# Performance work log

Hardware: AMD Instinct MI355X
Metric: run time of the kernel (lower is better)

## Reference

```python
import jax, jax.numpy as jnp
import numpy as np

N_NODES = 2048
N_FLUID = 400000
N_SOLID = 400000


def setup_inputs() -> dict:
    key = jax.random.key(0)
    k1, k2, k3 = jax.random.split(key, 3)
    nodes = jax.random.uniform(k1, (N_NODES, 3), dtype=jnp.float32)
    # sorted distinct node ids per tet: sort 4 draws from [0, N-4) then add offsets 0..3
    fe = jnp.sort(jax.random.randint(k2, (N_FLUID, 4), 0, N_NODES - 4), axis=1) + jnp.arange(4)
    se = jnp.sort(jax.random.randint(k3, (N_SOLID, 4), 0, N_NODES - 4), axis=1) + jnp.arange(4)
    return {
        "nodes": nodes,
        "fluid_elements": fe.astype(jnp.int32),
        "solid_elements": se.astype(jnp.int32),
        "E_mod": jnp.float32(2.1e11),
        "nu": jnp.float32(0.3),
        "rho_s": jnp.float32(7850.0),
    }


def _grads_and_volume(coords):
    """coords: [E,4,3] -> shape-fn gradients [E,4,3], volume [E]."""
    ones = jnp.ones(coords.shape[:-1] + (1,), coords.dtype)
    A = jnp.concatenate([ones, coords], axis=-1)
    A_inv = jnp.linalg.inv(A)
    grads = jnp.swapaxes(A_inv[..., 1:, :], -1, -2)        # [E,4,3]
    v0 = coords[:, 1] - coords[:, 0]
    v1 = coords[:, 2] - coords[:, 0]
    v2 = coords[:, 3] - coords[:, 0]
    vol = jnp.abs(jnp.linalg.det(jnp.stack([v0, v1, v2], axis=-1))) / 6.0  # [E]
    return grads, vol


def _fluid_element_matrices(coords):
    grads, vol = _grads_and_volume(coords)
    K_e = vol[:, None, None] * jnp.einsum("eik,ejk->eij", grads, grads)      # [E,4,4]
    m_template = (2.0 * jnp.eye(4, dtype=coords.dtype) + jnp.ones((4, 4), coords.dtype)) / 10.0
    M_e = vol[:, None, None] * m_template
    return K_e, M_e


def _elasticity_D(E_mod, nu):
    coeff = E_mod / ((1.0 + nu) * (1.0 - 2.0 * nu))
    top = nu * jnp.ones((3, 3), jnp.float32) + (1.0 - 2.0 * nu) * jnp.eye(3, dtype=jnp.float32)
    D = jnp.zeros((6, 6), jnp.float32)
    D = D.at[:3, :3].set(top)
    D = D.at[3:, 3:].set(((1.0 - 2.0 * nu) / 2.0) * jnp.eye(3, dtype=jnp.float32))
    return coeff * D


def _solid_element_matrices(coords, E_mod, nu, rho_s):
    grads, vol = _grads_and_volume(coords)                 # grads [E,4,3]
    bx, by, bz = grads[..., 0], grads[..., 1], grads[..., 2]   # each [E,4]
    z = jnp.zeros_like(bx)
    # per-node 6x3 strain-displacement block -> [E,4,6,3]
    block = jnp.stack([
        jnp.stack([bx, z, z], axis=-1),
        jnp.stack([z, by, z], axis=-1),
        jnp.stack([z, z, bz], axis=-1),
        jnp.stack([by, bx, z], axis=-1),
        jnp.stack([z, bz, by], axis=-1),
        jnp.stack([bz, z, bx], axis=-1),
    ], axis=-2)
    E = coords.shape[0]
    B = jnp.transpose(block, (0, 2, 1, 3)).reshape(E, 6, 12)  # [E,6,12]
    D = _elasticity_D(E_mod, nu)                              # [6,6]
    K_e = vol[:, None, None] * jnp.einsum("eai,ab,ebj->eij", B, D, B)  # [E,12,12]
    M_e = (rho_s * vol / 4.0)[:, None, None] * jnp.eye(12, dtype=coords.dtype)
    return K_e, M_e


def reference(nodes, fluid_elements, solid_elements, E_mod, nu, rho_s):
    n = nodes.shape[0]
    # ---- fluid: local matrices + scatter-add assembly into [N,N] ----
    cf = nodes[fluid_elements]                              # [Ef,4,3]
    Kf_e, Mf_e = _fluid_element_matrices(cf)
    rows = fluid_elements[:, :, None]                       # [Ef,4,1]
    cols = fluid_elements[:, None, :]                       # [Ef,1,4]
    K_f = jnp.zeros((n, n), jnp.float32).at[rows, cols].add(Kf_e)
    M_f = jnp.zeros((n, n), jnp.float32).at[rows, cols].add(Mf_e)
    # ---- solid: 3 dof/node, assembly into [3N,3N] ----
    cs = nodes[solid_elements]                              # [Es,4,3]
    Ks_e, Ms_e = _solid_element_matrices(cs, E_mod, nu, rho_s)
    dofs = (3 * solid_elements[:, :, None] + jnp.arange(3)).reshape(solid_elements.shape[0], 12)
    K_s = jnp.zeros((3 * n, 3 * n), jnp.float32).at[dofs[:, :, None], dofs[:, None, :]].add(Ks_e)
    M_s = jnp.zeros((3 * n, 3 * n), jnp.float32).at[dofs[:, :, None], dofs[:, None, :]].add(Ms_e)
    return (K_f, M_f, K_s, M_s)
```

## Files before the change

kernel.cpp:

```cpp
#include <hip/hip_runtime.h>


#define G_PART 256
#define BT 512
#define GW (BT / 64)
#define TCAP 1024
#define NCPT 4
#define VSTRIDE 13

__device__ __forceinline__ float sel4(float x0, float x1, float x2, float x3, int a) {
    float r = x0;
    r = (a == 1) ? x1 : r;
    r = (a == 2) ? x2 : r;
    r = (a == 3) ? x3 : r;
    return r;
}
__device__ __forceinline__ int sel4i(int x0, int x1, int x2, int x3, int a) {
    int r = x0;
    r = (a == 1) ? x1 : r;
    r = (a == 2) ? x2 : r;
    r = (a == 3) ? x3 : r;
    return r;
}

__device__ __forceinline__ float wave_reduce(float v) {
#pragma unroll
    for (int m = 1; m < 64; m <<= 1) v += __shfl_xor(v, m, 64);
    return v;
}

__device__ __forceinline__ void tet_geom_f(const float* __restrict__ nodes,
                                           int n0, int n1, int n2, int n3_,
                                           float& gx1, float& gy1, float& gz1,
                                           float& gx2, float& gy2, float& gz2,
                                           float& gx3, float& gy3, float& gz3,
                                           float& volf)
{
    const float* q0 = nodes + 3ll * n0;
    const float* q1 = nodes + 3ll * n1;
    const float* q2 = nodes + 3ll * n2;
    const float* q3 = nodes + 3ll * n3_;
    double p0x = q0[0], p0y = q0[1], p0z = q0[2];
    double r1x = (double)q1[0] - p0x, r1y = (double)q1[1] - p0y, r1z = (double)q1[2] - p0z;
    double r2x = (double)q2[0] - p0x, r2y = (double)q2[1] - p0y, r2z = (double)q2[2] - p0z;
    double r3x = (double)q3[0] - p0x, r3y = (double)q3[1] - p0y, r3z = (double)q3[2] - p0z;
    double c23x = r2y*r3z - r2z*r3y, c23y = r2z*r3x - r2x*r3z, c23z = r2x*r3y - r2y*r3x;
    double det = r1x*c23x + r1y*c23y + r1z*c23z;
    double inv = 1.0 / det;
    double c31x = r3y*r1z - r3z*r1y, c31y = r3z*r1x - r3x*r1z, c31z = r3x*r1y - r3y*r1x;
    double c12x = r1y*r2z - r1z*r2y, c12y = r1z*r2x - r1x*r2z, c12z = r1x*r2y - r1y*r2x;
    gx1 = (float)(c23x*inv); gy1 = (float)(c23y*inv); gz1 = (float)(c23z*inv);
    gx2 = (float)(c31x*inv); gy2 = (float)(c31y*inv); gz2 = (float)(c31z*inv);
    gx3 = (float)(c12x*inv); gy3 = (float)(c12y*inv); gz3 = (float)(c12z*inv);
    volf = (float)(fabs(det) / 6.0);
}

__device__ __forceinline__ int fetch_entry_bs(const int* __restrict__ ent,
                                              const int* __restrict__ Sb,
                                              const int* __restrict__ Qb,
                                              int chunk4, int v)
{
    int lo = 0, hi = 255;
#pragma unroll
    for (int it = 0; it < 8; ++it) {
        int mid = (lo + hi + 1) >> 1;
        bool ge = (Qb[mid] <= v);
        lo = ge ? mid : lo;
        hi = ge ? hi : mid - 1;
    }
    return ent[(size_t)lo * chunk4 + Sb[lo] + (v - Qb[lo])];
}

__global__ void __launch_bounds__(256)
index_build(const int4* __restrict__ fe, const int4* __restrict__ se,
            int* __restrict__ entF, int* __restrict__ entS,
            int* __restrict__ PF, int* __restrict__ PS,
            int nf, int ns, int n, int chunkF, int chunkS)
{
    extern __shared__ int h[];
    int* wsum = h + n;
    const bool solid = blockIdx.x >= G_PART;
    const int b = solid ? blockIdx.x - G_PART : blockIdx.x;
    const int4* elems = solid ? se : fe;
    const int nelem = solid ? ns : nf;
    const int chunk = solid ? chunkS : chunkF;
    int* P2 = solid ? PS : PF;
    int* entries = (solid ? entS : entF) + (size_t)b * 4 * chunk;

    const int t = threadIdx.x;
    const int beg = b * chunk, end = min(nelem, beg + chunk);

    for (int i = t; i < n; i += 256) h[i] = 0;
    __syncthreads();
    for (int e = beg + t; e < end; e += 256) {
        int4 nd = elems[e];
        atomicAdd(&h[nd.x], 1);
        atomicAdd(&h[nd.y], 1);
        atomicAdd(&h[nd.z], 1);
        atomicAdd(&h[nd.w], 1);
    }
    __syncthreads();

    const int cs = (n + 255) / 256;
    const int base = t * cs;
    int s = 0;
    for (int k = 0; k < cs; ++k) {
        int i = base + k;
        if (i < n) s += h[i];
    }
    wsum[t] = s;
    __syncthreads();
    for (int d = 1; d < 256; d <<= 1) {
        int v = (t >= d) ? wsum[t - d] : 0;
        __syncthreads();
        wsum[t] += v;
        __syncthreads();
    }
    int run = (t == 0) ? 0 : wsum[t - 1];
    for (int k = 0; k < cs; ++k) {
        int i = base + k;
        if (i < n) {
            int c = h[i]; h[i] = run;
            P2[(size_t)i * G_PART + b] = run;
            run += c;
        }
    }
    if (t == 255) P2[(size_t)n * G_PART + b] = wsum[255];
    __syncthreads();

    for (int e = beg + t; e < end; e += 256) {
        int4 nd = elems[e];
        int p;
        p = atomicAdd(&h[nd.x], 1); entries[p] = e * 4 + 0;
        p = atomicAdd(&h[nd.y], 1); entries[p] = e * 4 + 1;
        p = atomicAdd(&h[nd.z], 1); entries[p] = e * 4 + 2;
        p = atomicAdd(&h[nd.w], 1); entries[p] = e * 4 + 3;
    }
}

__global__ void __launch_bounds__(BT, 2)
fused_gather(const int* __restrict__ entF, const int* __restrict__ PF,
             const int* __restrict__ entS, const int* __restrict__ PS,
             const int4* __restrict__ fe, const int4* __restrict__ se,
             const float* __restrict__ nodes,
             float* __restrict__ Kf, float* __restrict__ Mf,
             float* __restrict__ Ks, float* __restrict__ Ms,
             const float* __restrict__ E_p, const float* __restrict__ nu_p,
             const float* __restrict__ rho_p, int n, int n3,
             int chunk4F, int chunk4S)
{
    extern __shared__ unsigned char smem[];
    float* vis  = (float*)smem;
    int*   pcnt = (int*)(vis + TCAP * VSTRIDE);
    int*   plist = pcnt + n;
    int*   Sb   = plist + 3 * TCAP;
    int*   Qb   = Sb + 256;
    int*   wsp  = Qb + 257;
    float* dred = (float*)(wsp + GW);

    const int tid = threadIdx.x;
    const int bid = blockIdx.x;
    const bool isSolid = bid < n;
    const int r = isSolid ? bid : bid - n;
    const int* ent = isSolid ? entS : entF;
    const int* P2  = isSolid ? PS : PF;
    const int4* elems4 = isSolid ? se : fe;
    const int chunk4 = isSolid ? chunk4S : chunk4F;

    if (tid < 256) {
        int s0 = P2[(size_t)r * G_PART + tid];
        int e0 = P2[(size_t)(r + 1) * G_PART + tid];
        Sb[tid] = s0;
        Qb[tid] = e0 - s0;
    }
    __syncthreads();
    if (tid < 64) {
        int c0 = Qb[4*tid], c1 = Qb[4*tid+1], c2 = Qb[4*tid+2], c3 = Qb[4*tid+3];
        int s = c0 + c1 + c2 + c3;
        int x = s;
#pragma unroll
        for (int d = 1; d < 64; d <<= 1) {
            int y = __shfl_up(x, d, 64);
            if (tid >= d) x += y;
        }
        int ex = x - s;
        Qb[4*tid] = ex; Qb[4*tid+1] = ex + c0;
        Qb[4*tid+2] = ex + c0 + c1; Qb[4*tid+3] = ex + c0 + c1 + c2;
        if (tid == 63) Qb[256] = ex + s;
    }
    __syncthreads();
    const int T = Qb[256];
    const bool fast = (T <= TCAP);
    int* entLds = plist;

    if (fast && tid < 256) {
        int q0 = Qb[tid], q1 = Qb[tid + 1];
        const int* src = ent + (size_t)tid * chunk4 + Sb[tid];
        for (int k = 0; k < q1 - q0; ++k) entLds[q0 + k] = src[k];
    }
    __syncthreads();

    const float E = *E_p, nu = *nu_p, rho = *rho_p;
    const float coeff = E / ((1.f + nu) * (1.f - 2.f * nu));
    const float lam = coeff * nu;
    const float mu  = coeff * (1.f - 2.f * nu) * 0.5f;

    if (isSolid) {
        float acc[NCPT][9];
#pragma unroll
        for (int k = 0; k < NCPT; ++k)
#pragma unroll
            for (int j = 0; j < 9; ++j) acc[k][j] = 0.f;
        float d00=0,d01=0,d02=0,d10=0,d11=0,d12=0,d20=0,d21=0,d22=0,vsum=0;

#define STAGE_S(v_, a_, nd_) do { \
            float g1x,g1y,g1z,g2x,g2y,g2z,g3x,g3y,g3z,vol; \
            tet_geom_f(nodes, (nd_).x, (nd_).y, (nd_).z, (nd_).w, \
                       g1x,g1y,g1z, g2x,g2y,g2z, g3x,g3y,g3z, vol); \
            float g0x = -(g1x+g2x+g3x), g0y = -(g1y+g2y+g3y), g0z = -(g1z+g2z+g3z); \
            float* V = vis + (v_) * VSTRIDE; \
            V[0]=g1x; V[1]=g1y; V[2]=g1z; V[3]=g2x; V[4]=g2y; V[5]=g2z; \
            V[6]=g3x; V[7]=g3y; V[8]=g3z; V[9]=vol; \
            ((int*)V)[10] = (nd_).x | ((nd_).y << 11) | ((a_) << 22); \
            ((int*)V)[11] = (nd_).z | ((nd_).w << 11); \
            float ga0 = sel4(g0x,g1x,g2x,g3x,(a_)); \
            float ga1 = sel4(g0y,g1y,g2y,g3y,(a_)); \
            float ga2 = sel4(g0z,g1z,g2z,g3z,(a_)); \
            { \
                float lv = lam*vol, mv = mu*vol, lm = lv+mv; \
                float mgg = mv*(ga0*ga0 + ga1*ga1 + ga2*ga2); \
                d00 += lm*ga0*ga0 + mgg; d01 += lm*ga0*ga1;       d02 += lm*ga0*ga2; \
                d10 += lm*ga1*ga0;       d11 += lm*ga1*ga1 + mgg; d12 += lm*ga1*ga2; \
                d20 += lm*ga2*ga0;       d21 += lm*ga2*ga1;       d22 += lm*ga2*ga2 + mgg; \
                vsum += vol; \
            } \
            _Pragma("unroll") \
            for (int s_ = 0; s_ < 3; ++s_) { \
                int b_ = s_ + ((s_ >= (a_)) ? 1 : 0); \
                int cb_ = sel4i((nd_).x, (nd_).y, (nd_).z, (nd_).w, b_); \
                atomicAdd(&pcnt[cb_], 1); \
            } \
        } while (0)

        for (int vb = 0; vb < T; vb += TCAP) {
            const int Tb = min(T - vb, TCAP);
            for (int c = tid; c < n; c += BT) pcnt[c] = 0;
            __syncthreads();

            {
                int v0 = tid, v1 = tid + BT;
                int pk0 = -1, pk1 = -1;
                if (v0 < Tb) pk0 = fast ? entLds[v0] : fetch_entry_bs(ent, Sb, Qb, chunk4, vb + v0);
                if (v1 < Tb) pk1 = fast ? entLds[v1] : fetch_entry_bs(ent, Sb, Qb, chunk4, vb + v1);
                int4 nd0 = make_int4(0,0,0,0), nd1 = make_int4(0,0,0,0);
                if (pk0 >= 0) nd0 = elems4[pk0 >> 2];
                if (pk1 >= 0) nd1 = elems4[pk1 >> 2];
                if (pk0 >= 0) { int a0 = pk0 & 3; STAGE_S(v0, a0, nd0); }
                if (pk1 >= 0) { int a1 = pk1 & 3; STAGE_S(v1, a1, nd1); }
            }
            __syncthreads();

            {
                const int cs = (n + BT - 1) / BT;
                int cb0 = tid * cs;
                int s = 0;
                for (int k = 0; k < cs; ++k) {
                    int i = cb0 + k;
                    if (i < n) s += pcnt[i];
                }
                int x = s;
#pragma unroll
                for (int d = 1; d < 64; d <<= 1) {
                    int y = __shfl_up(x, d, 64);
                    if ((tid & 63) >= d) x += y;
                }
                if ((tid & 63) == 63) wsp[tid >> 6] = x;
                __syncthreads();
                if (tid == 0) {
                    int run = 0;
                    for (int w = 0; w < GW; ++w) { int t_ = wsp[w]; wsp[w] = run; run += t_; }
                }
                __syncthreads();
                int ex = (x - s) + wsp[tid >> 6];
                for (int k = 0; k < cs; ++k) {
                    int i = cb0 + k;
                    if (i < n) { int c0 = pcnt[i]; pcnt[i] = ex; ex += c0; }
                }
            }
            __syncthreads();

            for (int v = tid; v < Tb; v += BT) {
                const float* V = vis + v * VSTRIDE;
                int w0 = ((const int*)V)[10], w1 = ((const int*)V)[11];
                int a = (w0 >> 22) & 3;
                int c0 = w0 & 2047, c1 = (w0 >> 11) & 2047;
                int c2 = w1 & 2047, c3 = (w1 >> 11) & 2047;
#pragma unroll
                for (int s = 0; s < 3; ++s) {
                    int b = s + ((s >= a) ? 1 : 0);
                    int cb = sel4i(c0, c1, c2, c3, b);
                    int p = atomicAdd(&pcnt[cb], 1);
                    plist[p] = (v << 4) | (a << 2) | b;
                }
            }
            __syncthreads();

#pragma unroll
            for (int k = 0; k < NCPT; ++k) {
                int c = tid + k * BT;
                if (c < n) {
                    int s0 = (c == 0) ? 0 : pcnt[c - 1];
                    int s1 = pcnt[c];
                    for (int p = s0; p < s1; ++p) {
                        int pe = plist[p];
                        int v = pe >> 4, a = (pe >> 2) & 3, b = pe & 3;
                        const float* V = vis + v * VSTRIDE;
                        float g1x=V[0],g1y=V[1],g1z=V[2],g2x=V[3],g2y=V[4],g2z=V[5],
                              g3x=V[6],g3y=V[7],g3z=V[8],vol=V[9];
                        float g0x=-(g1x+g2x+g3x), g0y=-(g1y+g2y+g3y), g0z=-(g1z+g2z+g3z);
                        float ga0=sel4(g0x,g1x,g2x,g3x,a);
                        float ga1=sel4(g0y,g1y,g2y,g3y,a);
                        float ga2=sel4(g0z,g1z,g2z,g3z,a);
                        float gb0=sel4(g0x,g1x,g2x,g3x,b);
                        float gb1=sel4(g0y,g1y,g2y,g3y,b);
                        float gb2=sel4(g0z,g1z,g2z,g3z,b);
                        float lv=lam*vol, mv=mu*vol;
                        float la0=lv*ga0, la1=lv*ga1, la2=lv*ga2;
                        float ma0=mv*ga0, ma1=mv*ga1, ma2=mv*ga2;
                        float mgg=mv*(ga0*gb0 + ga1*gb1 + ga2*gb2);
                        acc[k][0] += la0*gb0 + ma0*gb0 + mgg;
                        acc[k][1] += la0*gb1 + ma1*gb0;
                        acc[k][2] += la0*gb2 + ma2*gb0;
                        acc[k][3] += la1*gb0 + ma0*gb1;
                        acc[k][4] += la1*gb1 + ma1*gb1 + mgg;
                        acc[k][5] += la1*gb2 + ma2*gb1;
                        acc[k][6] += la2*gb0 + ma0*gb2;
                        acc[k][7] += la2*gb1 + ma1*gb2;
                        acc[k][8] += la2*gb2 + ma2*gb2 + mgg;
                    }
                }
            }
            __syncthreads();
        }

        d00=wave_reduce(d00); d01=wave_reduce(d01); d02=wave_reduce(d02);
        d10=wave_reduce(d10); d11=wave_reduce(d11); d12=wave_reduce(d12);
        d20=wave_reduce(d20); d21=wave_reduce(d21); d22=wave_reduce(d22);
        vsum=wave_reduce(vsum);
        if ((tid & 63) == 0) {
            int w = tid >> 6;
            dred[w*10+0]=d00; dred[w*10+1]=d01; dred[w*10+2]=d02;
            dred[w*10+3]=d10; dred[w*10+4]=d11; dred[w*10+5]=d12;
            dred[w*10+6]=d20; dred[w*10+7]=d21; dred[w*10+8]=d22;
            dred[w*10+9]=vsum;
        }
        __syncthreads();
        if (tid < 10) {
            float t_ = 0.f;
            for (int w = 0; w < GW; ++w) t_ += dred[w*10 + tid];
            dred[GW*10 + tid] = t_;
        }
        __syncthreads();

        float* plane = (float*)vis;
        const int q = n3 >> 2;
#pragma unroll
        for (int i = 0; i < 3; ++i) {
#pragma unroll
            for (int k = 0; k < NCPT; ++k) {
                int c = tid + k * BT;
                if (c < n) {
                    bool dg = (c == r);
                    plane[3*c+0] = acc[k][i*3+0] + (dg ? dred[GW*10 + i*3+0] : 0.f);
                    plane[3*c+1] = acc[k][i*3+1] + (dg ? dred[GW*10 + i*3+1] : 0.f);
                    plane[3*c+2] = acc[k][i*3+2] + (dg ? dred[GW*10 + i*3+2] : 0.f);
                }
            }
            __syncthreads();
            float4* dst = (float4*)(Ks + (size_t)(3*r + i) * n3);
            for (int t4 = tid; t4 < q; t4 += BT) dst[t4] = ((const float4*)plane)[t4];
            __syncthreads();
        }
        const float msdiag = rho * 0.25f * dred[GW*10 + 9];
        for (int k4 = tid; k4 < 3 * q; k4 += BT) {
            int i = (k4 >= q) + (k4 >= 2*q);
            int t4 = k4 - i * q;
            int dcol = 3*r + i;
            int base = t4 << 2;
            float4 w;
            w.x = (base + 0 == dcol) ? msdiag : 0.f;
            w.y = (base + 1 == dcol) ? msdiag : 0.f;
            w.z = (base + 2 == dcol) ? msdiag : 0.f;
            w.w = (base + 3 == dcol) ? msdiag : 0.f;
            ((float4*)(Ms + (size_t)(3*r + i) * n3))[t4] = w;
        }
    } else {
        float accK[NCPT], accM[NCPT];
#pragma unroll
        for (int k = 0; k < NCPT; ++k) { accK[k] = 0.f; accM[k] = 0.f; }
        float dK = 0.f, dM = 0.f;

#define STAGE_F(v_, a_, nd_) do { \
            float g1x,g1y,g1z,g2x,g2y,g2z,g3x,g3y,g3z,vol; \
            tet_geom_f(nodes, (nd_).x, (nd_).y, (nd_).z, (nd_).w, \
                       g1x,g1y,g1z, g2x,g2y,g2z, g3x,g3y,g3z, vol); \
            float g0x = -(g1x+g2x+g3x), g0y = -(g1y+g2y+g3y), g0z = -(g1z+g2z+g3z); \
            float* V = vis + (v_) * VSTRIDE; \
            V[0]=g1x; V[1]=g1y; V[2]=g1z; V[3]=g2x; V[4]=g2y; V[5]=g2z; \
            V[6]=g3x; V[7]=g3y; V[8]=g3z; V[9]=vol; \
            ((int*)V)[10] = (nd_).x | ((nd_).y << 11) | ((a_) << 22); \
            ((int*)V)[11] = (nd_).z | ((nd_).w << 11); \
            float ga0 = sel4(g0x,g1x,g2x,g3x,(a_)); \
            float ga1 = sel4(g0y,g1y,g2y,g3y,(a_)); \
            float ga2 = sel4(g0z,g1z,g2z,g3z,(a_)); \
            dK += vol*(ga0*ga0 + ga1*ga1 + ga2*ga2); \
            dM += vol*0.3f; \
            _Pragma("unroll") \
            for (int s_ = 0; s_ < 3; ++s_) { \
                int b_ = s_ + ((s_ >= (a_)) ? 1 : 0); \
                int cb_ = sel4i((nd_).x, (nd_).y, (nd_).z, (nd_).w, b_); \
                atomicAdd(&pcnt[cb_], 1); \
            } \
        } while (0)

        for (int vb = 0; vb < T; vb += TCAP) {
            const int Tb = min(T - vb, TCAP);
            for (int c = tid; c < n; c += BT) pcnt[c] = 0;
            __syncthreads();

            {
                int v0 = tid, v1 = tid + BT;
                int pk0 = -1, pk1 = -1;
                if (v0 < Tb) pk0 = fast ? entLds[v0] : fetch_entry_bs(ent, Sb, Qb, chunk4, vb + v0);
                if (v1 < Tb) pk1 = fast ? entLds[v1] : fetch_entry_bs(ent, Sb, Qb, chunk4, vb + v1);
                int4 nd0 = make_int4(0,0,0,0), nd1 = make_int4(0,0,0,0);
                if (pk0 >= 0) nd0 = elems4[pk0 >> 2];
                if (pk1 >= 0) nd1 = elems4[pk1 >> 2];
                if (pk0 >= 0) { int a0 = pk0 & 3; STAGE_F(v0, a0, nd0); }
                if (pk1 >= 0) { int a1 = pk1 & 3; STAGE_F(v1, a1, nd1); }
            }
            __syncthreads();

            {
                const int cs = (n + BT - 1) / BT;
                int cb0 = tid * cs;
                int s = 0;
                for (int k = 0; k < cs; ++k) {
                    int i = cb0 + k;
                    if (i < n) s += pcnt[i];
                }
                int x = s;
#pragma unroll
                for (int d = 1; d < 64; d <<= 1) {
                    int y = __shfl_up(x, d, 64);
                    if ((tid & 63) >= d) x += y;
                }
                if ((tid & 63) == 63) wsp[tid >> 6] = x;
                __syncthreads();
                if (tid == 0) {
                    int run = 0;
                    for (int w = 0; w < GW; ++w) { int t_ = wsp[w]; wsp[w] = run; run += t_; }
                }
                __syncthreads();
                int ex = (x - s) + wsp[tid >> 6];
                for (int k = 0; k < cs; ++k) {
                    int i = cb0 + k;
                    if (i < n) { int c0 = pcnt[i]; pcnt[i] = ex; ex += c0; }
                }
            }
            __syncthreads();

            for (int v = tid; v < Tb; v += BT) {
                const float* V = vis + v * VSTRIDE;
                int w0 = ((const int*)V)[10], w1 = ((const int*)V)[11];
                int a = (w0 >> 22) & 3;
                int c0 = w0 & 2047, c1 = (w0 >> 11) & 2047;
                int c2 = w1 & 2047, c3 = (w1 >> 11) & 2047;
#pragma unroll
                for (int s = 0; s < 3; ++s) {
                    int b = s + ((s >= a) ? 1 : 0);
                    int cb = sel4i(c0, c1, c2, c3, b);
                    int p = atomicAdd(&pcnt[cb], 1);
                    plist[p] = (v << 4) | (a << 2) | b;
                }
            }
            __syncthreads();

#pragma unroll
            for (int k = 0; k < NCPT; ++k) {
                int c = tid + k * BT;
                if (c < n) {
                    int s0 = (c == 0) ? 0 : pcnt[c - 1];
                    int s1 = pcnt[c];
                    for (int p = s0; p < s1; ++p) {
                        int pe = plist[p];
                        int v = pe >> 4, a = (pe >> 2) & 3, b = pe & 3;
                        const float* V = vis + v * VSTRIDE;
                        float g1x=V[0],g1y=V[1],g1z=V[2],g2x=V[3],g2y=V[4],g2z=V[5],
                              g3x=V[6],g3y=V[7],g3z=V[8],vol=V[9];
                        float g0x=-(g1x+g2x+g3x), g0y=-(g1y+g2y+g3y), g0z=-(g1z+g2z+g3z);
                        float ga0=sel4(g0x,g1x,g2x,g3x,a);
                        float ga1=sel4(g0y,g1y,g2y,g3y,a);
                        float ga2=sel4(g0z,g1z,g2z,g3z,a);
                        float gb0=sel4(g0x,g1x,g2x,g3x,b);
                        float gb1=sel4(g0y,g1y,g2y,g3y,b);
                        float gb2=sel4(g0z,g1z,g2z,g3z,b);
                        accK[k] += vol*(ga0*gb0 + ga1*gb1 + ga2*gb2);
                        accM[k] += vol*0.1f;
                    }
                }
            }
            __syncthreads();
        }

        dK = wave_reduce(dK);
        dM = wave_reduce(dM);
        if ((tid & 63) == 0) { int w = tid >> 6; dred[w*2+0] = dK; dred[w*2+1] = dM; }
        __syncthreads();
        if (tid < 2) {
            float t_ = 0.f;
            for (int w = 0; w < GW; ++w) t_ += dred[w*2 + tid];
            dred[GW*2 + tid] = t_;
        }
        __syncthreads();

#pragma unroll
        for (int k = 0; k < NCPT; ++k) {
            int c = tid + k * BT;
            if (c < n) {
                bool dg = (c == r);
                Kf[(size_t)r * n + c] = accK[k] + (dg ? dred[GW*2+0] : 0.f);
                Mf[(size_t)r * n + c] = accM[k] + (dg ? dred[GW*2+1] : 0.f);
            }
        }
    }
}

__device__ __forceinline__ void tet_grads_d(const float* __restrict__ nodes,
                                            const int* ni, double g[4][3], double& vol)
{
    double p[4][3];
#pragma unroll
    for (int a = 0; a < 4; ++a) {
        const float* q = nodes + 3ll * ni[a];
        p[a][0] = (double)q[0]; p[a][1] = (double)q[1]; p[a][2] = (double)q[2];
    }
    double r1[3], r2[3], r3[3];
#pragma unroll
    for (int k = 0; k < 3; ++k) {
        r1[k] = p[1][k] - p[0][k];
        r2[k] = p[2][k] - p[0][k];
        r3[k] = p[3][k] - p[0][k];
    }
    double c23[3] = { r2[1]*r3[2]-r2[2]*r3[1], r2[2]*r3[0]-r2[0]*r3[2], r2[0]*r3[1]-r2[1]*r3[0] };
    double det = r1[0]*c23[0] + r1[1]*c23[1] + r1[2]*c23[2];
    double inv = 1.0 / det;
    double c31[3] = { r3[1]*r1[2]-r3[2]*r1[1], r3[2]*r1[0]-r3[0]*r1[2], r3[0]*r1[1]-r3[1]*r1[0] };
    double c12[3] = { r1[1]*r2[2]-r1[2]*r2[1], r1[2]*r2[0]-r1[0]*r2[2], r1[0]*r2[1]-r1[1]*r2[0] };
#pragma unroll
    for (int k = 0; k < 3; ++k) {
        g[1][k] = c23[k]*inv; g[2][k] = c31[k]*inv; g[3][k] = c12[k]*inv;
        g[0][k] = -(g[1][k] + g[2][k] + g[3][k]);
    }
    vol = fabs(det) / 6.0;
}

__global__ void __launch_bounds__(256)
fluid_assemble(const float* __restrict__ nodes, const int* __restrict__ elems,
               float* __restrict__ Kf, float* __restrict__ Mf, int nelem, int n)
{
    int e = blockIdx.x * blockDim.x + threadIdx.x;
    if (e >= nelem) return;
    const int4 nd = *reinterpret_cast<const int4*>(elems + 4ll * e);
    int ni[4] = { nd.x, nd.y, nd.z, nd.w };
    double g[4][3], vol;
    tet_grads_d(nodes, ni, g, vol);
#pragma unroll
    for (int a = 0; a < 4; ++a) {
        long long rowoff = (long long)ni[a] * n;
#pragma unroll
        for (int b = 0; b < 4; ++b) {
            double kv = vol * (g[a][0]*g[b][0] + g[a][1]*g[b][1] + g[a][2]*g[b][2]);
            double mv = vol * (a == b ? 0.3 : 0.1);
            atomicAdd(Kf + rowoff + ni[b], (float)kv);
            atomicAdd(Mf + rowoff + ni[b], (float)mv);
        }
    }
}

__global__ void __launch_bounds__(256)
solid_assemble(const float* __restrict__ nodes, const int* __restrict__ elems,
               float* __restrict__ Ks, float* __restrict__ Ms,
               const float* __restrict__ E_p, const float* __restrict__ nu_p,
               const float* __restrict__ rho_p, int nelem, int n3)
{
    int e = blockIdx.x * blockDim.x + threadIdx.x;
    if (e >= nelem) return;
    double E = (double)*E_p, nu = (double)*nu_p, rho = (double)*rho_p;
    double coeff = E / ((1.0 + nu) * (1.0 - 2.0 * nu));
    double lam = coeff * nu, mu = coeff * (1.0 - 2.0 * nu) * 0.5;
    const int4 nd = *reinterpret_cast<const int4*>(elems + 4ll * e);
    int ni[4] = { nd.x, nd.y, nd.z, nd.w };
    double g[4][3], vol;
    tet_grads_d(nodes, ni, g, vol);
    double lv = lam * vol, mv = mu * vol;
#pragma unroll
    for (int a = 0; a < 4; ++a) {
        long long row0 = 3ll * ni[a];
#pragma unroll
        for (int b = 0; b < 4; ++b) {
            long long col0 = 3ll * ni[b];
            double gg = g[a][0]*g[b][0] + g[a][1]*g[b][1] + g[a][2]*g[b][2];
#pragma unroll
            for (int i = 0; i < 3; ++i) {
                float* rowp = Ks + (row0 + i) * (long long)n3 + col0;
#pragma unroll
                for (int j = 0; j < 3; ++j) {
                    double val = lv * g[a][i] * g[b][j] + mv * g[a][j] * g[b][i];
                    if (i == j) val += mv * gg;
                    atomicAdd(rowp + j, (float)val);
                }
            }
        }
        float mval = (float)(rho * vol * 0.25);
#pragma unroll
        for (int i = 0; i < 3; ++i) {
            long long d = row0 + i;
            atomicAdd(Ms + d * (long long)n3 + d, mval);
        }
    }
}

extern "C" void kernel_launch(void* const* d_in, const int* in_sizes, int n_in,
                              void* d_out, int out_size, void* d_ws, size_t ws_size,
                              hipStream_t stream)
{
    const float* nodes = (const float*)d_in[0];
    const int*   fe    = (const int*)d_in[1];
    const int*   se    = (const int*)d_in[2];
    const float* E_p   = (const float*)d_in[3];
    const float* nu_p  = (const float*)d_in[4];
    const float* rho_p = (const float*)d_in[5];

    const int n  = in_sizes[0] / 3;
    const int nf = in_sizes[1] / 4;
    const int ns = in_sizes[2] / 4;
    const int n3 = 3 * n;

    float* out = (float*)d_out;
    float* Kf = out;
    float* Mf = Kf + (size_t)n * n;
    float* Ks = Mf + (size_t)n * n;
    float* Ms = Ks + (size_t)n3 * n3;

    const int chunkF = (nf + G_PART - 1) / G_PART;
    const int chunkS = (ns + G_PART - 1) / G_PART;

    size_t pos = 0;
    auto take = [&](size_t bytes) {
        size_t p = pos;
        pos = (pos + bytes + 255) & ~(size_t)255;
        return p;
    };
    size_t entF_o = take((size_t)4 * chunkF * G_PART * 4);
    size_t entS_o = take((size_t)4 * chunkS * G_PART * 4);
    size_t PF_o   = take((size_t)(n + 1) * G_PART * 4);
    size_t PS_o   = take((size_t)(n + 1) * G_PART * 4);

    size_t gatherLds = (size_t)TCAP * VSTRIDE * 4 + (size_t)n * 4
                     + (size_t)3 * TCAP * 4 + (256 + 257 + GW) * 4
                     + (GW * 10 + 10) * 4;
    size_t indexLds  = (size_t)(n + 256) * 4;
    bool gather_ok = (pos <= ws_size) && (n <= 2048) && ((n & 3) == 0) &&
                     (n <= NCPT * BT) && (3 * n <= TCAP * VSTRIDE) &&
                     (gatherLds <= 80 * 1024) && (indexLds <= 64 * 1024);

    const int bs = 256;

    if (!gather_ok) {
        hipMemsetAsync(d_out, 0, (size_t)out_size * sizeof(float), stream);
        fluid_assemble<<<(nf + bs - 1) / bs, bs, 0, stream>>>(nodes, fe, Kf, Mf, nf, n);
        solid_assemble<<<(ns + bs - 1) / bs, bs, 0, stream>>>(nodes, se, Ks, Ms,
                                                              E_p, nu_p, rho_p, ns, n3);
        return;
    }

    char* ws = (char*)d_ws;
    int* entF = (int*)(ws + entF_o);
    int* entS = (int*)(ws + entS_o);
    int* PF   = (int*)(ws + PF_o);
    int* PS   = (int*)(ws + PS_o);

    const int4* fe4 = (const int4*)fe;
    const int4* se4 = (const int4*)se;

    index_build<<<2 * G_PART, bs, indexLds, stream>>>(fe4, se4, entF, entS, PF, PS,
                                                      nf, ns, n, chunkF, chunkS);
    fused_gather<<<2 * n, BT, gatherLds, stream>>>(entF, PF, entS, PS,
                                                   fe4, se4, nodes,
                                                   Kf, Mf, Ks, Ms,
                                                   E_p, nu_p, rho_p, n, n3,
                                                   4 * chunkF, 4 * chunkS);
}
```

Before: 191.8 us.

## Keep per-tet node ids in registers, drop LDS entry staging and plane writeback

Shrinks the per-tet LDS record from 13 to 11 floats by keeping the tet node ids and local index in registers for the scatter pass, instead of packing them into LDS and reading them back. Removes the LDS prestaging of the entry list, so entries are always fetched through the binary-search path. Replaces the LDS plane staging with coalesced float4 row writes of Ks/Ms by direct per-thread strided scalar stores, which removes several barriers but gives less coalesced global writes.

```diff
diff --git a/kernel.cpp b/kernel.cpp
--- a/kernel.cpp
+++ b/kernel.cpp
@@ -6,7 +6,7 @@
 #define GW (BT / 64)
 #define TCAP 1024
 #define NCPT 4
-#define VSTRIDE 13
+#define VSTRIDE 11
 
 __device__ __forceinline__ float sel4(float x0, float x1, float x2, float x3, int a) {
     float r = x0;
@@ -190,15 +190,6 @@
     }
     __syncthreads();
     const int T = Qb[256];
-    const bool fast = (T <= TCAP);
-    int* entLds = plist;
-
-    if (fast && tid < 256) {
-        int q0 = Qb[tid], q1 = Qb[tid + 1];
-        const int* src = ent + (size_t)tid * chunk4 + Sb[tid];
-        for (int k = 0; k < q1 - q0; ++k) entLds[q0 + k] = src[k];
-    }
-    __syncthreads();
 
     const float E = *E_p, nu = *nu_p, rho = *rho_p;
     const float coeff = E / ((1.f + nu) * (1.f - 2.f * nu));
@@ -213,51 +204,49 @@
             for (int j = 0; j < 9; ++j) acc[k][j] = 0.f;
         float d00=0,d01=0,d02=0,d10=0,d11=0,d12=0,d20=0,d21=0,d22=0,vsum=0;
 
+        for (int vb = 0; vb < T; vb += TCAP) {
+            const int Tb = min(T - vb, TCAP);
+            for (int c = tid; c < n; c += BT) pcnt[c] = 0;
+            __syncthreads();
+
+            const int v0 = tid, v1 = tid + BT;
+            const bool valid0 = v0 < Tb, valid1 = v1 < Tb;
+            int a0 = 0, a1 = 0;
+            int4 nd0 = make_int4(0,0,0,0), nd1 = make_int4(0,0,0,0);
+            if (valid0) {
+                int pk = fetch_entry_bs(ent, Sb, Qb, chunk4, vb + v0);
+                a0 = pk & 3; nd0 = elems4[pk >> 2];
+            }
+            if (valid1) {
+                int pk = fetch_entry_bs(ent, Sb, Qb, chunk4, vb + v1);
+                a1 = pk & 3; nd1 = elems4[pk >> 2];
+            }
 #define STAGE_S(v_, a_, nd_) do { \
-            float g1x,g1y,g1z,g2x,g2y,g2z,g3x,g3y,g3z,vol; \
-            tet_geom_f(nodes, (nd_).x, (nd_).y, (nd_).z, (nd_).w, \
-                       g1x,g1y,g1z, g2x,g2y,g2z, g3x,g3y,g3z, vol); \
-            float g0x = -(g1x+g2x+g3x), g0y = -(g1y+g2y+g3y), g0z = -(g1z+g2z+g3z); \
-            float* V = vis + (v_) * VSTRIDE; \
-            V[0]=g1x; V[1]=g1y; V[2]=g1z; V[3]=g2x; V[4]=g2y; V[5]=g2z; \
-            V[6]=g3x; V[7]=g3y; V[8]=g3z; V[9]=vol; \
-            ((int*)V)[10] = (nd_).x | ((nd_).y << 11) | ((a_) << 22); \
-            ((int*)V)[11] = (nd_).z | ((nd_).w << 11); \
-            float ga0 = sel4(g0x,g1x,g2x,g3x,(a_)); \
-            float ga1 = sel4(g0y,g1y,g2y,g3y,(a_)); \
-            float ga2 = sel4(g0z,g1z,g2z,g3z,(a_)); \
-            { \
+                float g1x,g1y,g1z,g2x,g2y,g2z,g3x,g3y,g3z,vol; \
+                tet_geom_f(nodes, (nd_).x, (nd_).y, (nd_).z, (nd_).w, \
+                           g1x,g1y,g1z, g2x,g2y,g2z, g3x,g3y,g3z, vol); \
+                float g0x = -(g1x+g2x+g3x), g0y = -(g1y+g2y+g3y), g0z = -(g1z+g2z+g3z); \
+                float* V = vis + (v_) * VSTRIDE; \
+                V[0]=g1x; V[1]=g1y; V[2]=g1z; V[3]=g2x; V[4]=g2y; V[5]=g2z; \
+                V[6]=g3x; V[7]=g3y; V[8]=g3z; V[9]=vol; \
+                float ga0 = sel4(g0x,g1x,g2x,g3x,(a_)); \
+                float ga1 = sel4(g0y,g1y,g2y,g3y,(a_)); \
+                float ga2 = sel4(g0z,g1z,g2z,g3z,(a_)); \
                 float lv = lam*vol, mv = mu*vol, lm = lv+mv; \
                 float mgg = mv*(ga0*ga0 + ga1*ga1 + ga2*ga2); \
                 d00 += lm*ga0*ga0 + mgg; d01 += lm*ga0*ga1;       d02 += lm*ga0*ga2; \
                 d10 += lm*ga1*ga0;       d11 += lm*ga1*ga1 + mgg; d12 += lm*ga1*ga2; \
                 d20 += lm*ga2*ga0;       d21 += lm*ga2*ga1;       d22 += lm*ga2*ga2 + mgg; \
                 vsum += vol; \
-            } \
-            _Pragma("unroll") \
-            for (int s_ = 0; s_ < 3; ++s_) { \
-                int b_ = s_ + ((s_ >= (a_)) ? 1 : 0); \
-                int cb_ = sel4i((nd_).x, (nd_).y, (nd_).z, (nd_).w, b_); \
-                atomicAdd(&pcnt[cb_], 1); \
-            } \
-        } while (0)
-
-        for (int vb = 0; vb < T; vb += TCAP) {
-            const int Tb = min(T - vb, TCAP);
-            for (int c = tid; c < n; c += BT) pcnt[c] = 0;
-            __syncthreads();
-
-            {
-                int v0 = tid, v1 = tid + BT;
-                int pk0 = -1, pk1 = -1;
-                if (v0 < Tb) pk0 = fast ? entLds[v0] : fetch_entry_bs(ent, Sb, Qb, chunk4, vb + v0);
-                if (v1 < Tb) pk1 = fast ? entLds[v1] : fetch_entry_bs(ent, Sb, Qb, chunk4, vb + v1);
-                int4 nd0 = make_int4(0,0,0,0), nd1 = make_int4(0,0,0,0);
-                if (pk0 >= 0) nd0 = elems4[pk0 >> 2];
-                if (pk1 >= 0) nd1 = elems4[pk1 >> 2];
-                if (pk0 >= 0) { int a0 = pk0 & 3; STAGE_S(v0, a0, nd0); }
-                if (pk1 >= 0) { int a1 = pk1 & 3; STAGE_S(v1, a1, nd1); }
-            }
+                _Pragma("unroll") \
+                for (int s_ = 0; s_ < 3; ++s_) { \
+                    int b_ = s_ + ((s_ >= (a_)) ? 1 : 0); \
+                    int cb_ = sel4i((nd_).x, (nd_).y, (nd_).z, (nd_).w, b_); \
+                    atomicAdd(&pcnt[cb_], 1); \
+                } \
+            } while (0)
+            if (valid0) STAGE_S(v0, a0, nd0);
+            if (valid1) STAGE_S(v1, a1, nd1);
             __syncthreads();
 
             {
@@ -289,20 +278,17 @@
             }
             __syncthreads();
 
-            for (int v = tid; v < Tb; v += BT) {
-                const float* V = vis + v * VSTRIDE;
-                int w0 = ((const int*)V)[10], w1 = ((const int*)V)[11];
-                int a = (w0 >> 22) & 3;
-                int c0 = w0 & 2047, c1 = (w0 >> 11) & 2047;
-                int c2 = w1 & 2047, c3 = (w1 >> 11) & 2047;
-#pragma unroll
-                for (int s = 0; s < 3; ++s) {
-                    int b = s + ((s >= a) ? 1 : 0);
-                    int cb = sel4i(c0, c1, c2, c3, b);
-                    int p = atomicAdd(&pcnt[cb], 1);
-                    plist[p] = (v << 4) | (a << 2) | b;
-                }
-            }
+#define SCAT(v_, a_, nd_) do { \
+                _Pragma("unroll") \
+                for (int s_ = 0; s_ < 3; ++s_) { \
+                    int b_ = s_ + ((s_ >= (a_)) ? 1 : 0); \
+                    int cb_ = sel4i((nd_).x, (nd_).y, (nd_).z, (nd_).w, b_); \
+                    int p_ = atomicAdd(&pcnt[cb_], 1); \
+                    plist[p_] = ((v_) << 4) | ((a_) << 2) | b_; \
+                } \
+            } while (0)
+            if (valid0) SCAT(v0, a0, nd0);
+            if (valid1) SCAT(v1, a1, nd1);
             __syncthreads();
 
 #pragma unroll
@@ -362,83 +348,77 @@
         }
         __syncthreads();
 
-        float* plane = (float*)vis;
-        const int q = n3 >> 2;
-#pragma unroll
-        for (int i = 0; i < 3; ++i) {
-#pragma unroll
-            for (int k = 0; k < NCPT; ++k) {
-                int c = tid + k * BT;
-                if (c < n) {
-                    bool dg = (c == r);
-                    plane[3*c+0] = acc[k][i*3+0] + (dg ? dred[GW*10 + i*3+0] : 0.f);
-                    plane[3*c+1] = acc[k][i*3+1] + (dg ? dred[GW*10 + i*3+1] : 0.f);
-                    plane[3*c+2] = acc[k][i*3+2] + (dg ? dred[GW*10 + i*3+2] : 0.f);
-                }
-            }
-            __syncthreads();
-            float4* dst = (float4*)(Ks + (size_t)(3*r + i) * n3);
-            for (int t4 = tid; t4 < q; t4 += BT) dst[t4] = ((const float4*)plane)[t4];
-            __syncthreads();
-        }
         const float msdiag = rho * 0.25f * dred[GW*10 + 9];
-        for (int k4 = tid; k4 < 3 * q; k4 += BT) {
-            int i = (k4 >= q) + (k4 >= 2*q);
-            int t4 = k4 - i * q;
-            int dcol = 3*r + i;
-            int base = t4 << 2;
-            float4 w;
-            w.x = (base + 0 == dcol) ? msdiag : 0.f;
-            w.y = (base + 1 == dcol) ? msdiag : 0.f;
-            w.z = (base + 2 == dcol) ? msdiag : 0.f;
-            w.w = (base + 3 == dcol) ? msdiag : 0.f;
-            ((float4*)(Ms + (size_t)(3*r + i) * n3))[t4] = w;
+#pragma unroll
+        for (int k = 0; k < NCPT; ++k) {
+            int c = tid + k * BT;
+            if (c < n) {
+                bool dg = (c == r);
+                float t0 = acc[k][0] + (dg ? dred[GW*10+0] : 0.f);
+                float t1 = acc[k][1] + (dg ? dred[GW*10+1] : 0.f);
+                float t2 = acc[k][2] + (dg ? dred[GW*10+2] : 0.f);
+                float t3 = acc[k][3] + (dg ? dred[GW*10+3] : 0.f);
+                float t4 = acc[k][4] + (dg ? dred[GW*10+4] : 0.f);
+                float t5 = acc[k][5] + (dg ? dred[GW*10+5] : 0.f);
+                float t6 = acc[k][6] + (dg ? dred[GW*10+6] : 0.f);
+                float t7 = acc[k][7] + (dg ? dred[GW*10+7] : 0.f);
+                float t8 = acc[k][8] + (dg ? dred[GW*10+8] : 0.f);
+                size_t ro0 = (size_t)(3*r + 0) * n3 + 3*c;
+                size_t ro1 = (size_t)(3*r + 1) * n3 + 3*c;
+                size_t ro2 = (size_t)(3*r + 2) * n3 + 3*c;
+                Ks[ro0+0]=t0; Ks[ro0+1]=t1; Ks[ro0+2]=t2;
+                Ks[ro1+0]=t3; Ks[ro1+1]=t4; Ks[ro1+2]=t5;
+                Ks[ro2+0]=t6; Ks[ro2+1]=t7; Ks[ro2+2]=t8;
+                Ms[ro0+0] = dg ? msdiag : 0.f; Ms[ro0+1] = 0.f; Ms[ro0+2] = 0.f;
+                Ms[ro1+0] = 0.f; Ms[ro1+1] = dg ? msdiag : 0.f; Ms[ro1+2] = 0.f;
+                Ms[ro2+0] = 0.f; Ms[ro2+1] = 0.f; Ms[ro2+2] = dg ? msdiag : 0.f;
+            }
         }
     } else {
         float accK[NCPT], accM[NCPT];
 #pragma unroll
         for (int k = 0; k < NCPT; ++k) { accK[k] = 0.f; accM[k] = 0.f; }
         float dK = 0.f, dM = 0.f;
-
-#define STAGE_F(v_, a_, nd_) do { \
-            float g1x,g1y,g1z,g2x,g2y,g2z,g3x,g3y,g3z,vol; \
-            tet_geom_f(nodes, (nd_).x, (nd_).y, (nd_).z, (nd_).w, \
-                       g1x,g1y,g1z, g2x,g2y,g2z, g3x,g3y,g3z, vol); \
-            float g0x = -(g1x+g2x+g3x), g0y = -(g1y+g2y+g3y), g0z = -(g1z+g2z+g3z); \
-            float* V = vis + (v_) * VSTRIDE; \
-            V[0]=g1x; V[1]=g1y; V[2]=g1z; V[3]=g2x; V[4]=g2y; V[5]=g2z; \
-            V[6]=g3x; V[7]=g3y; V[8]=g3z; V[9]=vol; \
-            ((int*)V)[10] = (nd_).x | ((nd_).y << 11) | ((a_) << 22); \
-            ((int*)V)[11] = (nd_).z | ((nd_).w << 11); \
-            float ga0 = sel4(g0x,g1x,g2x,g3x,(a_)); \
-            float ga1 = sel4(g0y,g1y,g2y,g3y,(a_)); \
-            float ga2 = sel4(g0z,g1z,g2z,g3z,(a_)); \
-            dK += vol*(ga0*ga0 + ga1*ga1 + ga2*ga2); \
-            dM += vol*0.3f; \
-            _Pragma("unroll") \
-            for (int s_ = 0; s_ < 3; ++s_) { \
-                int b_ = s_ + ((s_ >= (a_)) ? 1 : 0); \
-                int cb_ = sel4i((nd_).x, (nd_).y, (nd_).z, (nd_).w, b_); \
-                atomicAdd(&pcnt[cb_], 1); \
-            } \
-        } while (0)
 
         for (int vb = 0; vb < T; vb += TCAP) {
             const int Tb = min(T - vb, TCAP);
             for (int c = tid; c < n; c += BT) pcnt[c] = 0;
             __syncthreads();
 
-            {
-                int v0 = tid, v1 = tid + BT;
-                int pk0 = -1, pk1 = -1;
-                if (v0 < Tb) pk0 = fast ? entLds[v0] : fetch_entry_bs(ent, Sb, Qb, chunk4, vb + v0);
-                if (v1 < Tb) pk1 = fast ? entLds[v1] : fetch_entry_bs(ent, Sb, Qb, chunk4, vb + v1);
-                int4 nd0 = make_int4(0,0,0,0), nd1 = make_int4(0,0,0,0);
-                if (pk0 >= 0) nd0 = elems4[pk0 >> 2];
-                if (pk1 >= 0) nd1 = elems4[pk1 >> 2];
-                if (pk0 >= 0) { int a0 = pk0 & 3; STAGE_F(v0, a0, nd0); }
-                if (pk1 >= 0) { int a1 = pk1 & 3; STAGE_F(v1, a1, nd1); }
-            }
+            const int v0 = tid, v1 = tid + BT;
+            const bool valid0 = v0 < Tb, valid1 = v1 < Tb;
+            int a0 = 0, a1 = 0;
+            int4 nd0 = make_int4(0,0,0,0), nd1 = make_int4(0,0,0,0);
+            if (valid0) {
+                int pk = fetch_entry_bs(ent, Sb, Qb, chunk4, vb + v0);
+                a0 = pk & 3; nd0 = elems4[pk >> 2];
+            }
+            if (valid1) {
+                int pk = fetch_entry_bs(ent, Sb, Qb, chunk4, vb + v1);
+                a1 = pk & 3; nd1 = elems4[pk >> 2];
+            }
+#define STAGE_F(v_, a_, nd_) do { \
+                float g1x,g1y,g1z,g2x,g2y,g2z,g3x,g3y,g3z,vol; \
+                tet_geom_f(nodes, (nd_).x, (nd_).y, (nd_).z, (nd_).w, \
+                           g1x,g1y,g1z, g2x,g2y,g2z, g3x,g3y,g3z, vol); \
+                float g0x = -(g1x+g2x+g3x), g0y = -(g1y+g2y+g3y), g0z = -(g1z+g2z+g3z); \
+                float* V = vis + (v_) * VSTRIDE; \
+                V[0]=g1x; V[1]=g1y; V[2]=g1z; V[3]=g2x; V[4]=g2y; V[5]=g2z; \
+                V[6]=g3x; V[7]=g3y; V[8]=g3z; V[9]=vol; \
+                float ga0 = sel4(g0x,g1x,g2x,g3x,(a_)); \
+                float ga1 = sel4(g0y,g1y,g2y,g3y,(a_)); \
+                float ga2 = sel4(g0z,g1z,g2z,g3z,(a_)); \
+                dK += vol*(ga0*ga0 + ga1*ga1 + ga2*ga2); \
+                dM += vol*0.3f; \
+                _Pragma("unroll") \
+                for (int s_ = 0; s_ < 3; ++s_) { \
+                    int b_ = s_ + ((s_ >= (a_)) ? 1 : 0); \
+                    int cb_ = sel4i((nd_).x, (nd_).y, (nd_).z, (nd_).w, b_); \
+                    atomicAdd(&pcnt[cb_], 1); \
+                } \
+            } while (0)
+            if (valid0) STAGE_F(v0, a0, nd0);
+            if (valid1) STAGE_F(v1, a1, nd1);
             __syncthreads();
 
             {
@@ -470,20 +450,8 @@
             }
             __syncthreads();
 
-            for (int v = tid; v < Tb; v += BT) {
-                const float* V = vis + v * VSTRIDE;
-                int w0 = ((const int*)V)[10], w1 = ((const int*)V)[11];
-                int a = (w0 >> 22) & 3;
-                int c0 = w0 & 2047, c1 = (w0 >> 11) & 2047;
-                int c2 = w1 & 2047, c3 = (w1 >> 11) & 2047;
-#pragma unroll
-                for (int s = 0; s < 3; ++s) {
-                    int b = s + ((s >= a) ? 1 : 0);
-                    int cb = sel4i(c0, c1, c2, c3, b);
-                    int p = atomicAdd(&pcnt[cb], 1);
-                    plist[p] = (v << 4) | (a << 2) | b;
-                }
-            }
+            if (valid0) SCAT(v0, a0, nd0);
+            if (valid1) SCAT(v1, a1, nd1);
             __syncthreads();
 
 #pragma unroll
@@ -671,8 +639,7 @@
                      + (size_t)3 * TCAP * 4 + (256 + 257 + GW) * 4
                      + (GW * 10 + 10) * 4;
     size_t indexLds  = (size_t)(n + 256) * 4;
-    bool gather_ok = (pos <= ws_size) && (n <= 2048) && ((n & 3) == 0) &&
-                     (n <= NCPT * BT) && (3 * n <= TCAP * VSTRIDE) &&
+    bool gather_ok = (pos <= ws_size) && (n <= 2048) && (n <= NCPT * BT) &&
                      (gatherLds <= 80 * 1024) && (indexLds <= 64 * 1024);
 
     const int bs = 256;
```

Result: faster. 184.9 us (-3.6%).
